# Performance work log

Measured on AMD Instinct MI355X. Metric: run time of the kernel, lower is better.

Reference implementation:

```python
import jax, jax.numpy as jnp
import numpy as np

SLOPE = 25.0          # snntorch surrogate.fast_sigmoid default slope
ALPHA = 0.05          # attenuation_alpha

@jax.custom_vjp
def spike_fn(x):
    return (x > 0).astype(x.dtype)

def _spike_fwd(x):
    return (x > 0).astype(x.dtype), x

def _spike_bwd(x, g):
    return (g / (SLOPE * jnp.abs(x) + 1.0) ** 2,)

spike_fn.defvjp(_spike_fwd, _spike_bwd)

def lstm_cell(x, h, c, W_ih, W_hh, b_ih, b_hh):
    gates = x @ W_ih.T + b_ih + h @ W_hh.T + b_hh  # [B, 4H]
    i, f, g, o = jnp.split(gates, 4, axis=-1)
    i = jax.nn.sigmoid(i); f = jax.nn.sigmoid(f)
    g = jnp.tanh(g);       o = jax.nn.sigmoid(o)
    c_new = f * c + i * g
    h_new = o * jnp.tanh(c_new)
    return h_new, c_new

def slstm_step(x, syn, mem, W_ih, W_hh, b_ih, b_hh, thr):
    # reset is detached in snntorch (mem_reset -> .detach())
    reset = jax.lax.stop_gradient((mem > thr).astype(mem.dtype))
    h, c = lstm_cell(x, mem, syn, W_ih, W_hh, b_ih, b_hh)
    mem_new = h - reset * thr          # subtract reset mechanism
    spk = spike_fn(mem_new - thr)      # surrogate-gradient spike
    return spk, c, mem_new

def setup_inputs() -> dict:
    key = jax.random.key(0)
    ks = jax.random.split(key, 12)
    T, B, I, H, C = 512, 256, 14, 512, 8
    s = 0.05
    return {
        "x":     jax.random.normal(ks[0], (T, B, I), jnp.float32),
        "W_ih1": jax.random.normal(ks[1], (4 * H, I), jnp.float32) * s,
        "W_hh1": jax.random.normal(ks[2], (4 * H, H), jnp.float32) * s,
        "b_ih1": jax.random.normal(ks[3], (4 * H,), jnp.float32) * s,
        "b_hh1": jax.random.normal(ks[4], (4 * H,), jnp.float32) * s,
        "thr1":  jnp.ones((), jnp.float32),
        "W_ih2": jax.random.normal(ks[5], (4 * H, H), jnp.float32) * s,
        "W_hh2": jax.random.normal(ks[6], (4 * H, H), jnp.float32) * s,
        "b_ih2": jax.random.normal(ks[7], (4 * H,), jnp.float32) * s,
        "b_hh2": jax.random.normal(ks[8], (4 * H,), jnp.float32) * s,
        "thr2":  jnp.ones((), jnp.float32),
        "W_fc":  jax.random.normal(ks[9], (C, H), jnp.float32) * s,
        "b_fc":  jax.random.normal(ks[10], (C,), jnp.float32) * s,
    }

def reference(x, W_ih1, W_hh1, b_ih1, b_hh1, thr1,
              W_ih2, W_hh2, b_ih2, b_hh2, thr2, W_fc, b_fc):
    T, B, _ = x.shape
    H = W_hh1.shape[1]
    zeros = jnp.zeros((B, H), x.dtype)
    init = (zeros, zeros, zeros, zeros)  # syn1, mem1, syn2, mem2

    def step(carry, xt):
        syn1, mem1, syn2, mem2 = carry
        spk1, syn1, mem1 = slstm_step(xt, syn1, mem1, W_ih1, W_hh1, b_ih1, b_hh1, thr1)
        spk2, syn2, mem2 = slstm_step(spk1, syn2, mem2, W_ih2, W_hh2, b_ih2, b_hh2, thr2)
        return (syn1, mem1, syn2, mem2), mem2

    _, mem2_rec = jax.lax.scan(step, init, x)  # [T, B, H]

    t_idx = jnp.arange(T, 0, -1, dtype=x.dtype)
    w = jnp.exp(-ALPHA * (t_idx - 1.0))
    w = w / w.sum()
    final_mem = jnp.einsum('tbh,t->bh', mem2_rec, w)
    return final_mem @ W_fc.T + b_fc
```

## Files before the change

### kernel.cpp

```cpp
#include <hip/hip_runtime.h>


typedef _Float16 half8 __attribute__((ext_vector_type(8)));
typedef float    floatx4 __attribute__((ext_vector_type(4)));
typedef float    float2v __attribute__((ext_vector_type(2)));
typedef int      int4v  __attribute__((ext_vector_type(4)));

union H8 { int4v i; half8 h; };

#define T_STEPS 512
#define HDIM    512
#define ROWS    32
#define HSLICE  16
#define ACT_ELEMS 16384
#define WS_ACT_OFF 4096
#define WS_PART_OFF (WS_ACT_OFF + 2*5*8*ACT_ELEMS*2)
#define WS_PART_BYTES (256*32*8*4)
#define WS_MEMSET_BYTES WS_PART_OFF
#define PB_STRIDE 18

__device__ __forceinline__ float sigm(float v)  { return 1.0f/(1.0f + __expf(-v)); }
__device__ __forceinline__ float tanhf_(float v){ return 1.0f - 2.0f/(__expf(2.0f*v) + 1.0f); }
__device__ __forceinline__ void split16(float v, _Float16& h, _Float16& l) {
  h = (_Float16)v; l = (_Float16)(v - (float)h);
}
__device__ __forceinline__ unsigned pack2(_Float16 a, _Float16 b) {
  unsigned short ua = __builtin_bit_cast(unsigned short, a);
  unsigned short ub = __builtin_bit_cast(unsigned short, b);
  return (unsigned)ua | ((unsigned)ub << 16);
}

#define LDG16(dst, ptr) \
  asm volatile("global_load_dwordx4 %0, %1, off sc0 sc1" : "=v"((dst).i) : "v"(ptr) : "memory")

__device__ __forceinline__ void st_u32(unsigned* p, unsigned v) {
  __hip_atomic_store(p, v, __ATOMIC_RELAXED, __HIP_MEMORY_SCOPE_AGENT);
}

#define MFMA(A,B,C) __builtin_amdgcn_mfma_f32_16x16x32_f16((A),(B),(C),0,0,0)

__global__ __launch_bounds__(256) __attribute__((amdgpu_waves_per_eu(1, 1)))
void slstm_kernel(const float* __restrict__ x,
                  const float* __restrict__ Wih1, const float* __restrict__ Whh1,
                  const float* __restrict__ bih1, const float* __restrict__ bhh1,
                  const float* __restrict__ thr1p,
                  const float* __restrict__ Wih2, const float* __restrict__ Whh2,
                  const float* __restrict__ bih2, const float* __restrict__ bhh2,
                  const float* __restrict__ thr2p,
                  const float* __restrict__ Wfc,  const float* __restrict__ bfc,
                  float* __restrict__ out, unsigned char* __restrict__ ws)
{
  const int tid  = threadIdx.x;
  const int bid  = blockIdx.x;
  const int g    = bid & 7;
  const int cs   = bid >> 3;
  const int wave = tid >> 6;
  const int lane = tid & 63;
  const int l15  = lane & 15;
  const int lg   = lane >> 4;
  const int kr   = lg*8;

  __shared__ _Float16 wIloLds[4*16*64*8];
  __shared__ float    pbuf[4][128*PB_STRIDE + 16];
  __shared__ _Float16 xstage[ROWS*32];
  __shared__ float    b2s[64];

  unsigned* cntp  = (unsigned*)ws + (size_t)g*16;
  _Float16* actb  = (_Float16*)(ws + WS_ACT_OFF);
  float*    partb = (float*)(ws + WS_PART_OFF);

  half8 wAh[4][4], wAl[4][4], wIh[4][4], wHh[4][4], wHl[4][4];
#pragma unroll
  for (int q = 0; q < 4; ++q) {
    const int gcq = q*HDIM + cs*HSLICE + l15;
#pragma unroll
    for (int kl = 0; kl < 4; ++kl) {
      const int kb = wave*4 + kl;
      const float* p1 = Whh1 + (size_t)gcq*HDIM + kb*32 + kr;
      const float* p2 = Wih2 + (size_t)gcq*HDIM + kb*32 + kr;
      const float* p3 = Whh2 + (size_t)gcq*HDIM + kb*32 + kr;
      half8 ah, al, ih, il, hh, hl;
#pragma unroll
      for (int j = 0; j < 8; ++j) {
        _Float16 sh, sl;
        split16(p1[j], sh, sl); ah[j] = sh; al[j] = sl;
        split16(p2[j], sh, sl); ih[j] = sh; il[j] = sl;
        split16(p3[j], sh, sl); hh[j] = sh; hl[j] = sl;
      }
      wAh[q][kl] = ah; wAl[q][kl] = al; wIh[q][kl] = ih;
      wHh[q][kl] = hh; wHl[q][kl] = hl;
      *(half8*)&wIloLds[(((wave*4 + kl)*4 + q)*64 + lane)*8] = il;
    }
  }
  half8 wX1, wX2;
  {
    const int gcx = wave*HDIM + cs*HSLICE + l15;
#pragma unroll
    for (int j = 0; j < 8; ++j) {
      int k = kr + j;
      float v1 = 0.0f, v2 = 0.0f;
      _Float16 h, l;
      if (k < 14)       { split16(Wih1[(size_t)gcx*14 + k], h, l); v1 = (float)h; v2 = (float)l; }
      else if (k == 14) { split16(bih1[gcx] + bhh1[gcx], h, l); v1 = (float)h; }
      else if (k == 15) { split16(bih1[gcx] + bhh1[gcx], h, l); v1 = (float)l; }
      else if (k <= 29) { split16(Wih1[(size_t)gcx*14 + (k - 16)], h, l); v2 = (float)h; }
      wX1[j] = (_Float16)v1; wX2[j] = (_Float16)v2;
    }
  }
  if (tid < 64) {
    int q = tid >> 4, h = tid & 15;
    int gcl = q*HDIM + cs*HSLICE + h;
    b2s[tid] = bih2[gcl] + bhh2[gcl];
  }
  for (int idx = tid; idx < ROWS*32; idx += 256) {
    int k = idx & 31;
    if (k == 14 || k == 15) xstage[idx] = (_Float16)1.0f;
    else if (k >= 30)       xstage[idx] = (_Float16)0.0f;
  }
  __syncthreads();

  const float thr1 = thr1p[0], thr2 = thr2p[0];
  const int eb  = tid >> 3;
  const int ehl = (tid & 7)*2;
  const int ehg = cs*HSLICE + ehl;
  const int g16 = ((ehg >> 5)*2 + (eb >> 4))*64 + ((ehg >> 3) & 3)*16 + (eb & 15);
  const int u32i = g16*4 + ((ehg & 7) >> 1);
  const int r0 = tid/14,  k0 = tid%14;
  const int i1 = tid + 256;
  const int r1 = i1/14,   k1 = i1%14;

  float syn1[2] = {0,0}, m1p[2] = {0,0}, syn2[2] = {0,0}, m2p[2] = {0,0};
  float accf[2] = {0,0};
  const float invn = (1.0f - __expf(-0.05f)) / (1.0f - __expf(-0.05f*512.0f));
  int bar_dead = 0;

  size_t oA[4][2];
#pragma unroll
  for (int kl = 0; kl < 4; ++kl) {
    const int kb = wave*4 + kl;
    oA[kl][0] = (size_t)(((kb*2 + 0)*64 + lane)*16);
    oA[kl][1] = (size_t)(((kb*2 + 1)*64 + lane)*16);
  }

  H8 fh[4][2], fl[4][2];
  {
    const char* pH = (const char*)(actb + (size_t)((1*5 + 0)*8 + g)*ACT_ELEMS);
    const char* pL = (const char*)(actb + (size_t)((1*5 + 1)*8 + g)*ACT_ELEMS);
#pragma unroll
    for (int kl = 0; kl < 4; ++kl) {
      LDG16(fh[kl][0], pH + oA[kl][0]);  LDG16(fh[kl][1], pH + oA[kl][1]);
      LDG16(fl[kl][0], pL + oA[kl][0]);  LDG16(fl[kl][1], pL + oA[kl][1]);
    }
  }

  for (int t = 0; t < T_STEPS; ++t) {
    const int wp = t & 1, rp = wp ^ 1;

    const float* xt = x + ((size_t)t*256 + (size_t)g*ROWS)*14;
    { _Float16 h, l; split16(xt[r0*14 + k0], h, l);
      xstage[r0*32 + k0] = h; xstage[r0*32 + 16 + k0] = l; }
    if (i1 < 448) {
      _Float16 h, l; split16(xt[r1*14 + k1], h, l);
      xstage[r1*32 + k1] = h; xstage[r1*32 + 16 + k1] = l; }
    __syncthreads();

    floatx4 acc[4][2];
#pragma unroll
    for (int q = 0; q < 4; ++q) { acc[q][0] = (floatx4){0,0,0,0}; acc[q][1] = (floatx4){0,0,0,0}; }
    {
      half8 xa0 = *(const half8*)&xstage[l15*32 + kr];
      half8 xa1 = *(const half8*)&xstage[(16 + l15)*32 + kr];
      acc[wave][0] = MFMA(xa0, wX1, acc[wave][0]);  acc[wave][1] = MFMA(xa1, wX1, acc[wave][1]);
      acc[wave][0] = MFMA(xa0, wX2, acc[wave][0]);  acc[wave][1] = MFMA(xa1, wX2, acc[wave][1]);
    }
    asm volatile("s_waitcnt vmcnt(0)"
      : "+v"(fh[0][0].i), "+v"(fh[0][1].i), "+v"(fl[0][0].i), "+v"(fl[0][1].i),
        "+v"(fh[1][0].i), "+v"(fh[1][1].i), "+v"(fl[1][0].i), "+v"(fl[1][1].i),
        "+v"(fh[2][0].i), "+v"(fh[2][1].i), "+v"(fl[2][0].i), "+v"(fl[2][1].i),
        "+v"(fh[3][0].i), "+v"(fh[3][1].i), "+v"(fl[3][0].i), "+v"(fl[3][1].i)
      : : "memory");
#pragma unroll
    for (int kl = 0; kl < 4; ++kl)
#pragma unroll
      for (int q = 0; q < 4; ++q) {
        acc[q][0] = MFMA(fh[kl][0].h, wAh[q][kl], acc[q][0]);
        acc[q][1] = MFMA(fh[kl][1].h, wAh[q][kl], acc[q][1]);
        acc[q][0] = MFMA(fh[kl][0].h, wAl[q][kl], acc[q][0]);
        acc[q][1] = MFMA(fh[kl][1].h, wAl[q][kl], acc[q][1]);
        acc[q][0] = MFMA(fl[kl][0].h, wAh[q][kl], acc[q][0]);
        acc[q][1] = MFMA(fl[kl][1].h, wAh[q][kl], acc[q][1]);
      }
#pragma unroll
    for (int q = 0; q < 4; ++q)
#pragma unroll
      for (int tl = 0; tl < 2; ++tl)
#pragma unroll
        for (int p = 0; p < 4; ++p)
          pbuf[wave][(q*32 + tl*16 + lg*4 + p)*PB_STRIDE + l15] = acc[q][tl][p];
    __syncthreads();

    {
      unsigned* m1hW = (unsigned*)(actb + (size_t)((wp*5 + 0)*8 + g)*ACT_ELEMS);
      unsigned* m1lW = (unsigned*)(actb + (size_t)((wp*5 + 1)*8 + g)*ACT_ELEMS);
      unsigned* spW  = (unsigned*)(actb + (size_t)((wp*5 + 2)*8 + g)*ACT_ELEMS);
      float2v pi2 = {0,0}, pf2 = {0,0}, pg2 = {0,0}, po2 = {0,0};
#pragma unroll
      for (int w = 0; w < 4; ++w) {
        pi2 += *(const float2v*)&pbuf[w][(0*32 + eb)*PB_STRIDE + ehl];
        pf2 += *(const float2v*)&pbuf[w][(1*32 + eb)*PB_STRIDE + ehl];
        pg2 += *(const float2v*)&pbuf[w][(2*32 + eb)*PB_STRIDE + ehl];
        po2 += *(const float2v*)&pbuf[w][(3*32 + eb)*PB_STRIDE + ehl];
      }
      _Float16 mh[2], ml[2], sp[2];
#pragma unroll
      for (int c = 0; c < 2; ++c) {
        float iv = sigm(pi2[c]), fv = sigm(pf2[c]), gv = tanhf_(pg2[c]), ov = sigm(po2[c]);
        float cnew = fv*syn1[c] + iv*gv;
        syn1[c] = cnew;
        float hnew = ov*tanhf_(cnew);
        float m1 = hnew - ((m1p[c] > thr1) ? thr1 : 0.0f);
        m1p[c] = m1;
        split16(m1, mh[c], ml[c]);
        sp[c] = ((m1 - thr1) > 0.0f) ? (_Float16)1.0f : (_Float16)0.0f;
      }
      st_u32(m1hW + u32i, pack2(mh[0], mh[1]));
      st_u32(m1lW + u32i, pack2(ml[0], ml[1]));
      st_u32(spW  + u32i, pack2(sp[0], sp[1]));
    }

    asm volatile("s_waitcnt vmcnt(0)" ::: "memory");
    __syncthreads();
    if (tid == 0 && !bar_dead) {
      __hip_atomic_fetch_add(cntp, 1u, __ATOMIC_RELAXED, __HIP_MEMORY_SCOPE_AGENT);
      unsigned target = 32u*(unsigned)(t + 1);
      int tries = 0;
      while (__hip_atomic_load(cntp, __ATOMIC_RELAXED, __HIP_MEMORY_SCOPE_AGENT) < target) {
        __builtin_amdgcn_s_sleep(1);
        if (++tries > (1 << 20)) { bar_dead = 1; break; }
      }
    }
    __syncthreads();
    __atomic_signal_fence(__ATOMIC_SEQ_CST);

    const char* baseS  = (const char*)(actb + (size_t)((wp*5 + 2)*8 + g)*ACT_ELEMS);
    const char* base2H = (const char*)(actb + (size_t)((rp*5 + 3)*8 + g)*ACT_ELEMS);
    const char* base2L = (const char*)(actb + (size_t)((rp*5 + 4)*8 + g)*ACT_ELEMS);
    const char* nH = (const char*)(actb + (size_t)((wp*5 + 0)*8 + g)*ACT_ELEMS);
    const char* nL = (const char*)(actb + (size_t)((wp*5 + 1)*8 + g)*ACT_ELEMS);
#pragma unroll
    for (int q = 0; q < 4; ++q) { acc[q][0] = (floatx4){0,0,0,0}; acc[q][1] = (floatx4){0,0,0,0}; }

    H8 sb[2][2], mbh[2][2], mbl[2][2];
#pragma unroll
    for (int kc = 0; kc < 2; ++kc) {
      LDG16(sb[kc][0],  baseS  + oA[kc][0]);  LDG16(sb[kc][1],  baseS  + oA[kc][1]);
      LDG16(mbh[kc][0], base2H + oA[kc][0]);  LDG16(mbh[kc][1], base2H + oA[kc][1]);
      LDG16(mbl[kc][0], base2L + oA[kc][0]);  LDG16(mbl[kc][1], base2L + oA[kc][1]);
    }
    asm volatile("s_waitcnt vmcnt(0)"
      : "+v"(sb[0][0].i), "+v"(sb[0][1].i), "+v"(mbh[0][0].i), "+v"(mbh[0][1].i),
        "+v"(mbl[0][0].i), "+v"(mbl[0][1].i),
        "+v"(sb[1][0].i), "+v"(sb[1][1].i), "+v"(mbh[1][0].i), "+v"(mbh[1][1].i),
        "+v"(mbl[1][0].i), "+v"(mbl[1][1].i)
      : : "memory");
#pragma unroll
    for (int kc = 0; kc < 2; ++kc) {
      const int kl = kc;
#pragma unroll
      for (int q = 0; q < 4; ++q) {
        half8 wIl = *(const half8*)&wIloLds[(((wave*4 + kl)*4 + q)*64 + lane)*8];
        acc[q][0] = MFMA(sb[kc][0].h,  wIh[q][kl], acc[q][0]);
        acc[q][1] = MFMA(sb[kc][1].h,  wIh[q][kl], acc[q][1]);
        acc[q][0] = MFMA(sb[kc][0].h,  wIl,        acc[q][0]);
        acc[q][1] = MFMA(sb[kc][1].h,  wIl,        acc[q][1]);
        acc[q][0] = MFMA(mbh[kc][0].h, wHh[q][kl], acc[q][0]);
        acc[q][1] = MFMA(mbh[kc][1].h, wHh[q][kl], acc[q][1]);
        acc[q][0] = MFMA(mbh[kc][0].h, wHl[q][kl], acc[q][0]);
        acc[q][1] = MFMA(mbh[kc][1].h, wHl[q][kl], acc[q][1]);
        acc[q][0] = MFMA(mbl[kc][0].h, wHh[q][kl], acc[q][0]);
        acc[q][1] = MFMA(mbl[kc][1].h, wHh[q][kl], acc[q][1]);
      }
    }
#pragma unroll
    for (int kc = 0; kc < 2; ++kc) {
      LDG16(sb[kc][0],  baseS  + oA[2+kc][0]);  LDG16(sb[kc][1],  baseS  + oA[2+kc][1]);
      LDG16(mbh[kc][0], base2H + oA[2+kc][0]);  LDG16(mbh[kc][1], base2H + oA[2+kc][1]);
      LDG16(mbl[kc][0], base2L + oA[2+kc][0]);  LDG16(mbl[kc][1], base2L + oA[2+kc][1]);
    }
#pragma unroll
    for (int kl = 0; kl < 4; ++kl) {
      LDG16(fh[kl][0], nH + oA[kl][0]);  LDG16(fh[kl][1], nH + oA[kl][1]);
      LDG16(fl[kl][0], nL + oA[kl][0]);  LDG16(fl[kl][1], nL + oA[kl][1]);
    }
    asm volatile("s_waitcnt vmcnt(16)"
      : "+v"(sb[0][0].i), "+v"(sb[0][1].i), "+v"(mbh[0][0].i), "+v"(mbh[0][1].i),
        "+v"(mbl[0][0].i), "+v"(mbl[0][1].i),
        "+v"(sb[1][0].i), "+v"(sb[1][1].i), "+v"(mbh[1][0].i), "+v"(mbh[1][1].i),
        "+v"(mbl[1][0].i), "+v"(mbl[1][1].i)
      : : "memory");
#pragma unroll
    for (int kc = 0; kc < 2; ++kc) {
      const int kl = 2 + kc;
#pragma unroll
      for (int q = 0; q < 4; ++q) {
        half8 wIl = *(const half8*)&wIloLds[(((wave*4 + kl)*4 + q)*64 + lane)*8];
        acc[q][0] = MFMA(sb[kc][0].h,  wIh[q][kl], acc[q][0]);
        acc[q][1] = MFMA(sb[kc][1].h,  wIh[q][kl], acc[q][1]);
        acc[q][0] = MFMA(sb[kc][0].h,  wIl,        acc[q][0]);
        acc[q][1] = MFMA(sb[kc][1].h,  wIl,        acc[q][1]);
        acc[q][0] = MFMA(mbh[kc][0].h, wHh[q][kl], acc[q][0]);
        acc[q][1] = MFMA(mbh[kc][1].h, wHh[q][kl], acc[q][1]);
        acc[q][0] = MFMA(mbh[kc][0].h, wHl[q][kl], acc[q][0]);
        acc[q][1] = MFMA(mbh[kc][1].h, wHl[q][kl], acc[q][1]);
        acc[q][0] = MFMA(mbl[kc][0].h, wHh[q][kl], acc[q][0]);
        acc[q][1] = MFMA(mbl[kc][1].h, wHh[q][kl], acc[q][1]);
      }
    }
#pragma unroll
    for (int q = 0; q < 4; ++q)
#pragma unroll
      for (int tl = 0; tl < 2; ++tl)
#pragma unroll
        for (int p = 0; p < 4; ++p)
          pbuf[wave][(q*32 + tl*16 + lg*4 + p)*PB_STRIDE + l15] = acc[q][tl][p];
    __syncthreads();

    float wt = __expf(0.05f*(float)(t + 1 - T_STEPS)) * invn;
    {
      unsigned* m2hW = (unsigned*)(actb + (size_t)((wp*5 + 3)*8 + g)*ACT_ELEMS);
      unsigned* m2lW = (unsigned*)(actb + (size_t)((wp*5 + 4)*8 + g)*ACT_ELEMS);
      float2v pi2, pf2, pg2, po2;
      pi2 = *(const float2v*)&b2s[0*16 + ehl];
      pf2 = *(const float2v*)&b2s[1*16 + ehl];
      pg2 = *(const float2v*)&b2s[2*16 + ehl];
      po2 = *(const float2v*)&b2s[3*16 + ehl];
#pragma unroll
      for (int w = 0; w < 4; ++w) {
        pi2 += *(const float2v*)&pbuf[w][(0*32 + eb)*PB_STRIDE + ehl];
        pf2 += *(const float2v*)&pbuf[w][(1*32 + eb)*PB_STRIDE + ehl];
        pg2 += *(const float2v*)&pbuf[w][(2*32 + eb)*PB_STRIDE + ehl];
        po2 += *(const float2v*)&pbuf[w][(3*32 + eb)*PB_STRIDE + ehl];
      }
      _Float16 mh[2], ml[2];
#pragma unroll
      for (int c = 0; c < 2; ++c) {
        float iv = sigm(pi2[c]), fv = sigm(pf2[c]), gv = tanhf_(pg2[c]), ov = sigm(po2[c]);
        float cnew = fv*syn2[c] + iv*gv;
        syn2[c] = cnew;
        float hnew = ov*tanhf_(cnew);
        float m2 = hnew - ((m2p[c] > thr2) ? thr2 : 0.0f);
        m2p[c] = m2;
        accf[c] += wt * m2;
        split16(m2, mh[c], ml[c]);
      }
      st_u32(m2hW + u32i, pack2(mh[0], mh[1]));
      st_u32(m2lW + u32i, pack2(ml[0], ml[1]));
    }
  }

  float part[8];
#pragma unroll
  for (int c = 0; c < 8; ++c)
    part[c] = accf[0]*Wfc[c*HDIM + ehg] + accf[1]*Wfc[c*HDIM + ehg + 1];
#pragma unroll
  for (int off = 1; off < 8; off <<= 1)
#pragma unroll
    for (int c = 0; c < 8; ++c)
      part[c] += __shfl_xor(part[c], off, 64);
  {
    int c = tid & 7;
    __hip_atomic_store(&partb[((size_t)(g*32 + cs)*32 + (size_t)eb)*8 + c], part[c],
                       __ATOMIC_RELAXED, __HIP_MEMORY_SCOPE_AGENT);
  }
  asm volatile("s_waitcnt vmcnt(0)" ::: "memory");
  __syncthreads();
  if (tid == 0 && !bar_dead) {
    __hip_atomic_fetch_add(cntp, 1u, __ATOMIC_RELAXED, __HIP_MEMORY_SCOPE_AGENT);
    unsigned target = 32u*513u;
    int tries = 0;
    while (__hip_atomic_load(cntp, __ATOMIC_RELAXED, __HIP_MEMORY_SCOPE_AGENT) < target) {
      __builtin_amdgcn_s_sleep(1);
      if (++tries > (1 << 20)) break;
    }
  }
  __syncthreads();
  __atomic_signal_fence(__ATOMIC_SEQ_CST);

  if (cs == 0) {
    int b = tid >> 3, c = tid & 7;
    float s = bfc[c];
#pragma unroll 4
    for (int jj = 0; jj < 32; ++jj)
      s += __hip_atomic_load(&partb[((size_t)(g*32 + jj)*32 + (size_t)b)*8 + c],
                             __ATOMIC_RELAXED, __HIP_MEMORY_SCOPE_AGENT);
    out[(g*ROWS + b)*8 + c] = s;
  }
}

extern "C" void kernel_launch(void* const* d_in, const int* in_sizes, int n_in,
                              void* d_out, int out_size, void* d_ws, size_t ws_size,
                              hipStream_t stream) {
  (void)in_sizes; (void)n_in;
  const float* x    = (const float*)d_in[0];
  const float* Wih1 = (const float*)d_in[1];
  const float* Whh1 = (const float*)d_in[2];
  const float* bih1 = (const float*)d_in[3];
  const float* bhh1 = (const float*)d_in[4];
  const float* thr1 = (const float*)d_in[5];
  const float* Wih2 = (const float*)d_in[6];
  const float* Whh2 = (const float*)d_in[7];
  const float* bih2 = (const float*)d_in[8];
  const float* bhh2 = (const float*)d_in[9];
  const float* thr2 = (const float*)d_in[10];
  const float* Wfc  = (const float*)d_in[11];
  const float* bfc  = (const float*)d_in[12];
  float* out = (float*)d_out;
  unsigned char* ws = (unsigned char*)d_ws;

  if (ws_size < (size_t)(WS_PART_OFF + WS_PART_BYTES)) {
    hipError_t e1 = hipMemsetAsync(d_out, 0x7f, (size_t)out_size*4, stream);
    (void)e1;
    return;
  }
  hipError_t e2 = hipMemsetAsync(d_ws, 0, WS_MEMSET_BYTES, stream);
  (void)e2;

  slstm_kernel<<<dim3(256), dim3(256), 0, stream>>>(
      x, Wih1, Whh1, bih1, bhh1, thr1,
      Wih2, Whh2, bih2, bhh2, thr2, Wfc, bfc, out, ws);
}
```

Before: 4.855 ms.

## Replace atomic counter barrier with per-block flag array polled by every wave

Replaces the per-group atomic fetch-add counter barrier with a flag array where each of the 32 blocks in a group stores its step number. Every wave polls all 32 flags in parallel with one load per lane and a ballot, which removes the atomic RMW contention, the s_sleep backoff and the second __syncthreads on every timestep. The cost is more polling traffic from every wave. Memory ordering now relies on each wave observing the flags directly, and the spin limit is lower.

New measurement: 4.866 ms. About the same (+0.2%).

```diff
diff --git a/kernel.cpp b/kernel.cpp
--- a/kernel.cpp
+++ b/kernel.cpp
@@ -13,6 +13,7 @@
 #define ROWS    32
 #define HSLICE  16
 #define ACT_ELEMS 16384
+#define WS_FLAG_OFF 1024
 #define WS_ACT_OFF 4096
 #define WS_PART_OFF (WS_ACT_OFF + 2*5*8*ACT_ELEMS*2)
 #define WS_PART_BYTES (256*32*8*4)
@@ -65,7 +66,7 @@
   __shared__ _Float16 xstage[ROWS*32];
   __shared__ float    b2s[64];
 
-  unsigned* cntp  = (unsigned*)ws + (size_t)g*16;
+  unsigned* flagp = (unsigned*)(ws + WS_FLAG_OFF) + (size_t)g*32;
   _Float16* actb  = (_Float16*)(ws + WS_ACT_OFF);
   float*    partb = (float*)(ws + WS_PART_OFF);
 
@@ -230,16 +231,17 @@
 
     asm volatile("s_waitcnt vmcnt(0)" ::: "memory");
     __syncthreads();
-    if (tid == 0 && !bar_dead) {
-      __hip_atomic_fetch_add(cntp, 1u, __ATOMIC_RELAXED, __HIP_MEMORY_SCOPE_AGENT);
-      unsigned target = 32u*(unsigned)(t + 1);
+    const unsigned target = (unsigned)(t + 1);
+    if (tid == 0) st_u32(flagp + cs, target);
+    if (!bar_dead) {
       int tries = 0;
-      while (__hip_atomic_load(cntp, __ATOMIC_RELAXED, __HIP_MEMORY_SCOPE_AGENT) < target) {
-        __builtin_amdgcn_s_sleep(1);
-        if (++tries > (1 << 20)) { bar_dead = 1; break; }
-      }
-    }
-    __syncthreads();
+      for (;;) {
+        unsigned v = __hip_atomic_load(&flagp[lane & 31], __ATOMIC_RELAXED,
+                                       __HIP_MEMORY_SCOPE_AGENT);
+        if (__ballot(v < target) == 0ull) break;
+        if (++tries > (1 << 18)) { bar_dead = 1; break; }
+      }
+    }
     __atomic_signal_fence(__ATOMIC_SEQ_CST);
 
     const char* baseS  = (const char*)(actb + (size_t)((wp*5 + 2)*8 + g)*ACT_ELEMS);
@@ -374,16 +376,19 @@
   }
   asm volatile("s_waitcnt vmcnt(0)" ::: "memory");
   __syncthreads();
-  if (tid == 0 && !bar_dead) {
-    __hip_atomic_fetch_add(cntp, 1u, __ATOMIC_RELAXED, __HIP_MEMORY_SCOPE_AGENT);
-    unsigned target = 32u*513u;
-    int tries = 0;
-    while (__hip_atomic_load(cntp, __ATOMIC_RELAXED, __HIP_MEMORY_SCOPE_AGENT) < target) {
-      __builtin_amdgcn_s_sleep(1);
-      if (++tries > (1 << 20)) break;
-    }
-  }
-  __syncthreads();
+  {
+    const unsigned target = (unsigned)(T_STEPS + 1);
+    if (tid == 0) st_u32(flagp + cs, target);
+    if (!bar_dead) {
+      int tries = 0;
+      for (;;) {
+        unsigned v = __hip_atomic_load(&flagp[lane & 31], __ATOMIC_RELAXED,
+                                       __HIP_MEMORY_SCOPE_AGENT);
+        if (__ballot(v < target) == 0ull) break;
+        if (++tries > (1 << 18)) break;
+      }
+    }
+  }
   __atomic_signal_fence(__ATOMIC_SEQ_CST);
 
   if (cs == 0) {
```
